# Performance work log

Measured on AMD Instinct MI355X. Metric: run time of the kernel, lower is better.

## Reference

```python
import jax, jax.numpy as jnp
import numpy as np

B, S, D, H, F = 2, 2048, 2048, 16, 6144
HD = D // H  # 128
EPS = 1e-5
NEG = -1e9


def layernorm(x, g, b):
    m = jnp.mean(x, axis=-1, keepdims=True)
    v = jnp.var(x, axis=-1, keepdims=True)
    return (x - m) * jax.lax.rsqrt(v + EPS) * g + b


def setup_inputs() -> dict:
    key = jax.random.key(0)
    ks = jax.random.split(key, 16)
    w = 0.02
    hidden_states = jax.random.normal(ks[0], (B, S, D), jnp.float32)
    # additive causal mask [B,1,S,S]
    causal = jnp.tril(jnp.ones((S, S), jnp.bool_))
    attention_mask = jnp.broadcast_to(jnp.where(causal, 0.0, NEG).astype(jnp.float32)[None, None], (B, 1, S, S))
    # ALiBi position bias [H,S,S]
    slopes = 2.0 ** (-8.0 * (jnp.arange(1, H + 1, dtype=jnp.float32)) / H)
    rel = (jnp.arange(S)[None, :] - jnp.arange(S)[:, None]).astype(jnp.float32)  # j - i (<=0 causal)
    position_bias = slopes[:, None, None] * rel[None]
    params = dict(
        ln1_g=jnp.ones((D,), jnp.float32), ln1_b=jnp.zeros((D,), jnp.float32),
        w_qkv=jax.random.normal(ks[1], (D, 3 * D), jnp.float32) * w,
        b_qkv=jnp.zeros((3 * D,), jnp.float32),
        w_o=jax.random.normal(ks[2], (D, D), jnp.float32) * w,
        b_o=jnp.zeros((D,), jnp.float32),
        ln2_g=jnp.ones((D,), jnp.float32), ln2_b=jnp.zeros((D,), jnp.float32),
        w_fc=jax.random.normal(ks[3], (D, F), jnp.float32) * w,
        b_fc=jnp.zeros((F,), jnp.float32),
        w_fc2=jax.random.normal(ks[4], (D, F), jnp.float32) * w,
        b_fc2=jnp.zeros((F,), jnp.float32),
        w_proj=jax.random.normal(ks[5], (F, D), jnp.float32) * w,
        b_proj=jnp.zeros((D,), jnp.float32),
    )
    return dict(hidden_states=hidden_states, attention_mask=attention_mask,
                position_bias=position_bias, **params)


def reference(hidden_states, attention_mask, position_bias,
              ln1_g, ln1_b, w_qkv, b_qkv, w_o, b_o,
              ln2_g, ln2_b, w_fc, b_fc, w_fc2, b_fc2, w_proj, b_proj):
    residual = hidden_states
    h = layernorm(hidden_states, ln1_g, ln1_b)
    qkv = h @ w_qkv + b_qkv  # [B,S,3D]
    q, k, v = jnp.split(qkv, 3, axis=-1)
    # split heads -> [B,H,S,HD]
    def heads(t):
        return t.reshape(B, S, H, HD).transpose(0, 2, 1, 3)
    q, k, v = heads(q), heads(k), heads(v)
    # muP scaling: attn_scale_power=1.0 -> divide by head_dim
    scores = jnp.einsum('bhqd,bhkd->bhqk', q, k) / jnp.float32(HD)
    scores = scores + attention_mask + position_bias[None]
    probs = jax.nn.softmax(scores, axis=-1)
    ctx = jnp.einsum('bhqk,bhkd->bhqd', probs, v)
    ctx = ctx.transpose(0, 2, 1, 3).reshape(B, S, D)
    attn_out = ctx @ w_o + b_o
    hidden = attn_out + residual
    # SwiGLU MLP
    residual = hidden
    h2 = layernorm(hidden, ln2_g, ln2_b)
    gate = h2 @ w_fc2 + b_fc2
    up = h2 @ w_fc + b_fc
    mlp = (up * jax.nn.silu(gate)) @ w_proj + b_proj
    return mlp + residual
```

## Files before the change

kernel.cpp:

```cpp
#include <hip/hip_runtime.h>
#include <hip/hip_bf16.h>
#include <math.h>

#define DI __device__ __forceinline__

typedef __bf16 bf16x8 __attribute__((ext_vector_type(8)));
typedef float f32x4 __attribute__((ext_vector_type(4)));
typedef short s16x8 __attribute__((ext_vector_type(8)));

DI unsigned short f2bf(float f) {
  unsigned int u = __builtin_bit_cast(unsigned int, f);
  unsigned int r = (u + 0x7fffu + ((u >> 16) & 1u)) >> 16;
  return (unsigned short)r;
}
DI float bf2f(unsigned short h) {
  unsigned int u = ((unsigned int)h) << 16;
  return __builtin_bit_cast(float, u);
}

DI void gload16(const void* g, void* l) {
  __builtin_amdgcn_global_load_lds(
      (const __attribute__((address_space(1))) void*)g,
      (__attribute__((address_space(3))) void*)l, 16, 0, 0);
}

DI unsigned ldsoff(const void* p) {
  return (unsigned)(size_t)(const __attribute__((address_space(3))) void*)p;
}

template <int OFF>
DI bf16x8 ds128(unsigned base) {
  bf16x8 r;
  asm volatile("ds_read_b128 %0, %1 offset:%2" : "=v"(r) : "v"(base), "i"(OFF));
  return r;
}
template <int N>
DI void lgkm() {
  asm volatile("s_waitcnt lgkmcnt(%0)" ::"i"(N));
  __builtin_amdgcn_sched_barrier(0);
}
template <int N>
DI void vmc() {
  asm volatile("s_waitcnt vmcnt(%0)" ::"i"(N));
  __builtin_amdgcn_sched_barrier(0);
}

DI void xcd_map(int BN, int& m0, int& n0) {
  const int nx = gridDim.x;
  int orig = blockIdx.y * nx + blockIdx.x;
  int xcd = orig & 7, k = orig >> 3;
  int xm = xcd >> 2, xn = xcd & 3;
  int nband = nx >> 2;
  m0 = (xm * 8 + (k & 7)) * 256;
  n0 = (xn * nband + (k >> 3)) * BN;
}

__global__ __launch_bounds__(256)
void transpose_cast_f32(const float* __restrict__ in, unsigned short* __restrict__ out,
                        int R, int C) {
  __shared__ unsigned int t[64 * 65];
  const int r0 = blockIdx.y * 64, c0 = blockIdx.x * 64;
  const int tid = threadIdx.x;
#pragma unroll
  for (int p = 0; p < 4; ++p) {
    int e = p * 1024 + tid * 4;
    int r = e >> 6, c = e & 63;
    float4 v = *(const float4*)(in + (size_t)(r0 + r) * C + c0 + c);
    t[r * 65 + c + 0] = f2bf(v.x);
    t[r * 65 + c + 1] = f2bf(v.y);
    t[r * 65 + c + 2] = f2bf(v.z);
    t[r * 65 + c + 3] = f2bf(v.w);
  }
  __syncthreads();
  const int oc = tid >> 2, ch = tid & 3;
  alignas(16) unsigned short vals[16];
#pragma unroll
  for (int j = 0; j < 16; ++j) vals[j] = (unsigned short)t[(ch * 16 + j) * 65 + oc];
  size_t ob = (size_t)(c0 + oc) * R + r0 + ch * 16;
  *(s16x8*)(out + ob) = *(const s16x8*)(vals);
  *(s16x8*)(out + ob + 8) = *(const s16x8*)(vals + 8);
}

__global__ __launch_bounds__(256)
void transpose_v(const unsigned short* __restrict__ qkv, unsigned short* __restrict__ vT) {
  __shared__ unsigned int t[64 * 65];
  const int s0 = blockIdx.x * 64, d0 = blockIdx.y * 64, bh = blockIdx.z;
  const int b = bh >> 4, h = bh & 15;
  const int tid = threadIdx.x;
#pragma unroll
  for (int p = 0; p < 2; ++p) {
    int id = p * 256 + tid;
    int r = id >> 3, c = (id & 7) * 8;
    s16x8 v = *(const s16x8*)(qkv + (size_t)(b * 2048 + s0 + r) * 6144 + 4096 + h * 128 + d0 + c);
#pragma unroll
    for (int j = 0; j < 8; ++j) t[r * 65 + c + j] = (unsigned short)((const unsigned short*)&v)[j];
  }
  __syncthreads();
  const int oc = tid >> 2, ch = tid & 3;
  alignas(16) unsigned short vals[16];
#pragma unroll
  for (int j = 0; j < 16; ++j) vals[j] = (unsigned short)t[(ch * 16 + j) * 65 + oc];
  size_t ob = (size_t)(bh * 128 + d0 + oc) * 2048 + s0 + ch * 16;
  *(s16x8*)(vT + ob) = *(const s16x8*)(vals);
  *(s16x8*)(vT + ob + 8) = *(const s16x8*)(vals + 8);
}

__global__ __launch_bounds__(256)
void ln_kernel(const float* __restrict__ x, const float* __restrict__ g,
               const float* __restrict__ bi, unsigned short* __restrict__ y) {
  __shared__ float red[8];
  const int row = blockIdx.x, tid = threadIdx.x;
  const float* xp = x + (size_t)row * 2048 + tid * 8;
  float4 v0 = *(const float4*)xp;
  float4 v1 = *(const float4*)(xp + 4);
  float v[8] = {v0.x, v0.y, v0.z, v0.w, v1.x, v1.y, v1.z, v1.w};
  float s = 0.f;
#pragma unroll
  for (int j = 0; j < 8; ++j) s += v[j];
#pragma unroll
  for (int d = 1; d < 64; d <<= 1) s += __shfl_xor(s, d);
  if ((tid & 63) == 0) red[tid >> 6] = s;
  __syncthreads();
  float mean = (red[0] + red[1] + red[2] + red[3]) * (1.f / 2048.f);
  float dd[8], sq = 0.f;
#pragma unroll
  for (int j = 0; j < 8; ++j) { dd[j] = v[j] - mean; sq += dd[j] * dd[j]; }
#pragma unroll
  for (int d = 1; d < 64; d <<= 1) sq += __shfl_xor(sq, d);
  if ((tid & 63) == 0) red[4 + (tid >> 6)] = sq;
  __syncthreads();
  float var = (red[4] + red[5] + red[6] + red[7]) * (1.f / 2048.f);
  float rs = rsqrtf(var + 1e-5f);
  float4 g0 = *(const float4*)(g + tid * 8), g1 = *(const float4*)(g + tid * 8 + 4);
  float4 b0 = *(const float4*)(bi + tid * 8), b1 = *(const float4*)(bi + tid * 8 + 4);
  float gg[8] = {g0.x, g0.y, g0.z, g0.w, g1.x, g1.y, g1.z, g1.w};
  float bb[8] = {b0.x, b0.y, b0.z, b0.w, b1.x, b1.y, b1.z, b1.w};
  alignas(16) unsigned short o[8];
#pragma unroll
  for (int j = 0; j < 8; ++j) o[j] = f2bf(dd[j] * rs * gg[j] + bb[j]);
  *(s16x8*)(y + (size_t)row * 2048 + tid * 8) = *(const s16x8*)o;
}

DI void stage_half(const unsigned short* __restrict__ G, int ld, int rbase, int kt,
                   int h, unsigned short* dst, int tid) {
#pragma unroll
  for (int i = 0; i < 2; ++i) {
    int id = i * 512 + tid;
    int rl = id >> 3, sl = id & 7;
    int ss = sl ^ (rl & 7);
    gload16(G + (size_t)(rbase + h * 128 + rl) * ld + kt + ss * 8,
            (char*)dst + h * 16384 + id * 16);
  }
}

#define RDA(dst, B0_, B1_, OFS)                                        \
  dst[0][0] = ds128<(OFS) + 0>(B0_);    dst[0][1] = ds128<(OFS) + 0>(B1_);    \
  dst[1][0] = ds128<(OFS) + 2048>(B0_); dst[1][1] = ds128<(OFS) + 2048>(B1_); \
  dst[2][0] = ds128<(OFS) + 4096>(B0_); dst[2][1] = ds128<(OFS) + 4096>(B1_); \
  dst[3][0] = ds128<(OFS) + 6144>(B0_); dst[3][1] = ds128<(OFS) + 6144>(B1_);

#define RDB(dst, B0_, B1_, OFS)                                        \
  dst[0][0] = ds128<(OFS) + 0>(B0_);    dst[0][1] = ds128<(OFS) + 0>(B1_);    \
  dst[1][0] = ds128<(OFS) + 2048>(B0_); dst[1][1] = ds128<(OFS) + 2048>(B1_);

template <int MODE>
__global__ __launch_bounds__(512, 2)
void gemm256(const unsigned short* __restrict__ A, int lda,
             const unsigned short* __restrict__ B,
             const float* __restrict__ bias,
             const void* __restrict__ resg,
             void* __restrict__ out, int ldc, int K) {
  __shared__ alignas(16) unsigned short As[2][256 * 64];
  __shared__ alignas(16) unsigned short Bs[2][256 * 64];

  const int tid = threadIdx.x;
  const int l = tid & 63, w = tid >> 6;
  const int wr = w >> 2, wc = w & 3;
  const int lr = l & 15, lg = l >> 4;

  int m0, n0;
  xcd_map(256, m0, n0);

  const int NT = K >> 6;

  f32x4 acc[8][4];
  const f32x4 z4 = {0.f, 0.f, 0.f, 0.f};
#pragma unroll
  for (int i = 0; i < 8; ++i)
#pragma unroll
    for (int j = 0; j < 4; ++j) acc[i][j] = z4;

  const int s7 = lr & 7;
  const unsigned swz0 = (unsigned)((lg ^ s7) << 4);
  const unsigned swz1 = (unsigned)(((4 | lg) ^ s7) << 4);
  const unsigned rA = (unsigned)((wr * 128 + lr) * 128);
  const unsigned rB = (unsigned)((wc * 64 + lr) * 128);
  const unsigned aA0 = ldsoff(&As[0][0]) + rA + swz0;
  const unsigned aA1 = ldsoff(&As[0][0]) + rA + swz1;
  const unsigned bA0 = ldsoff(&Bs[0][0]) + rB + swz0;
  const unsigned bA1 = ldsoff(&Bs[0][0]) + rB + swz1;

  stage_half(A, lda, m0, 0, 0, As[0], tid);
  stage_half(A, lda, m0, 0, 1, As[0], tid);
  stage_half(B, K, n0, 0, 0, Bs[0], tid);
  stage_half(B, K, n0, 0, 1, Bs[0], tid);
  if (NT > 1) {
    stage_half(B, K, n0, 64, 0, Bs[1], tid);
    stage_half(B, K, n0, 64, 1, Bs[1], tid);
    stage_half(A, lda, m0, 64, 0, As[1], tid);
    asm volatile("s_waitcnt vmcnt(6)" ::: "memory");
  } else {
    asm volatile("s_waitcnt vmcnt(0)" ::: "memory");
  }
  __builtin_amdgcn_s_barrier();

  for (int t = 0; t < NT; ++t) {
    const unsigned co = (unsigned)((t & 1) * 32768);
    const unsigned a0b = aA0 + co, a1b = aA1 + co;
    const unsigned b0b = bA0 + co, b1b = bA1 + co;
    bf16x8 a0[4][2], a1[4][2], bfr[4][2];

#pragma unroll
    for (int i = 0; i < 4; ++i) {
      a0[i][0] = ds128<0>(a0b + i * 2048);
      a0[i][1] = ds128<0>(a1b + i * 2048);
    }
#pragma unroll
    for (int j = 0; j < 2; ++j) {
      bfr[j][0] = ds128<0>(b0b + j * 2048);
      bfr[j][1] = ds128<0>(b1b + j * 2048);
    }
    if (t + 1 < NT) stage_half(A, lda, m0, (t + 1) * 64, 1, As[(t & 1) ^ 1], tid);
#pragma unroll
    for (int j = 2; j < 4; ++j) {
      bfr[j][0] = ds128<0>(b0b + j * 2048);
      bfr[j][1] = ds128<0>(b1b + j * 2048);
    }
    lgkm<4>();
    __builtin_amdgcn_s_setprio(1);
#pragma unroll
    for (int i = 0; i < 4; ++i)
#pragma unroll
      for (int j = 0; j < 2; ++j)
#pragma unroll
        for (int kk = 0; kk < 2; ++kk)
          acc[i][j] = __builtin_amdgcn_mfma_f32_16x16x32_bf16(a0[i][kk], bfr[j][kk], acc[i][j], 0, 0, 0);
    __builtin_amdgcn_s_setprio(0);
    __builtin_amdgcn_s_barrier();

#pragma unroll
    for (int i = 0; i < 4; ++i) {
      a1[i][0] = ds128<8192>(a0b + i * 2048);
      a1[i][1] = ds128<8192>(a1b + i * 2048);
    }
    lgkm<8>();
    __builtin_amdgcn_s_setprio(1);
#pragma unroll
    for (int i = 0; i < 4; ++i)
#pragma unroll
      for (int j = 2; j < 4; ++j)
#pragma unroll
        for (int kk = 0; kk < 2; ++kk)
          acc[i][j] = __builtin_amdgcn_mfma_f32_16x16x32_bf16(a0[i][kk], bfr[j][kk], acc[i][j], 0, 0, 0);
    __builtin_amdgcn_s_setprio(0);
    __builtin_amdgcn_s_barrier();

    if (t + 2 < NT) stage_half(B, K, n0, (t + 2) * 64, 0, Bs[t & 1], tid);
    lgkm<0>();
    __builtin_amdgcn_s_setprio(1);
#pragma unroll
    for (int i = 0; i < 4; ++i)
#pragma unroll
      for (int j = 0; j < 2; ++j)
#pragma unroll
        for (int kk = 0; kk < 2; ++kk)
          acc[i + 4][j] = __builtin_amdgcn_mfma_f32_16x16x32_bf16(a1[i][kk], bfr[j][kk], acc[i + 4][j], 0, 0, 0);
    __builtin_amdgcn_s_setprio(0);
    __builtin_amdgcn_s_barrier();

    if (t + 2 < NT) {
      stage_half(B, K, n0, (t + 2) * 64, 1, Bs[t & 1], tid);
      stage_half(A, lda, m0, (t + 2) * 64, 0, As[t & 1], tid);
    }
    __builtin_amdgcn_s_setprio(1);
#pragma unroll
    for (int i = 0; i < 4; ++i)
#pragma unroll
      for (int j = 2; j < 4; ++j)
#pragma unroll
        for (int kk = 0; kk < 2; ++kk)
          acc[i + 4][j] = __builtin_amdgcn_mfma_f32_16x16x32_bf16(a1[i][kk], bfr[j][kk], acc[i + 4][j], 0, 0, 0);
    __builtin_amdgcn_s_setprio(0);
    if (t + 2 < NT) { vmc<6>(); } else { vmc<0>(); }
    __builtin_amdgcn_s_barrier();
  }

#pragma unroll
  for (int i = 0; i < 8; ++i) {
    int r0 = m0 + wr * 128 + i * 16 + lg * 4;
#pragma unroll
    for (int j = 0; j < 4; ++j) {
      int col = n0 + wc * 64 + j * 16 + lr;
      float bb = bias[col];
#pragma unroll
      for (int q = 0; q < 4; ++q) {
        size_t off = (size_t)(r0 + q) * ldc + col;
        float v = acc[i][j][q] + bb;
        if (MODE == 0) {
          ((unsigned short*)out)[off] = f2bf(v);
        } else {
          ((float*)out)[off] = v + ((const float*)resg)[off];
        }
      }
    }
  }
}

template <int MODE, bool DUAL>
__global__ __launch_bounds__(512, 2)
void gemm_n128(const unsigned short* __restrict__ A, int lda,
               const unsigned short* __restrict__ B0,
               const unsigned short* __restrict__ B1,
               const float* __restrict__ bias0, const float* __restrict__ bias1,
               const void* __restrict__ resg,
               void* __restrict__ out, int ldc, int K) {
  __shared__ alignas(16) unsigned short As[2][256 * 64];
  __shared__ alignas(16) unsigned short Bs0[2][128 * 64];

  const int tid = threadIdx.x;
  const int l = tid & 63, w = tid >> 6;
  const int wr = w >> 2, wc = w & 3;
  const int lr = l & 15, lg = l >> 4;

  int m0, n0;
  xcd_map(128, m0, n0);

  const int NT = K >> 6;

  f32x4 acc0[8][2];
  const f32x4 z4 = {0.f, 0.f, 0.f, 0.f};
#pragma unroll
  for (int i = 0; i < 8; ++i)
#pragma unroll
    for (int j = 0; j < 2; ++j) acc0[i][j] = z4;

  const int s7 = lr & 7;
  const unsigned swz0 = (unsigned)((lg ^ s7) << 4);
  const unsigned swz1 = (unsigned)(((4 | lg) ^ s7) << 4);
  const unsigned rA = (unsigned)((wr * 128 + lr) * 128);
  const unsigned rB = (unsigned)((wc * 32 + lr) * 128);
  const unsigned aA0 = ldsoff(&As[0][0]) + rA + swz0;
  const unsigned aA1 = ldsoff(&As[0][0]) + rA + swz1;
  const unsigned bA0 = ldsoff(&Bs0[0][0]) + rB + swz0;
  const unsigned bA1 = ldsoff(&Bs0[0][0]) + rB + swz1;

  stage_half(A, lda, m0, 0, 0, As[0], tid);
  stage_half(A, lda, m0, 0, 1, As[0], tid);
  stage_half(B0, K, n0, 0, 0, Bs0[0], tid);
  if (NT > 1) {
    stage_half(B0, K, n0, 64, 0, Bs0[1], tid);
    stage_half(A, lda, m0, 64, 0, As[1], tid);
    asm volatile("s_waitcnt vmcnt(4)" ::: "memory");
  } else {
    asm volatile("s_waitcnt vmcnt(0)" ::: "memory");
  }
  __builtin_amdgcn_s_barrier();

  for (int t = 0; t < NT; ++t) {
    const int cur = t & 1;
    const unsigned ca = aA0 + (unsigned)(cur * 32768);
    const unsigned ca1 = aA1 + (unsigned)(cur * 32768);
    const unsigned cb = bA0 + (unsigned)(cur * 16384);
    const unsigned cb1 = bA1 + (unsigned)(cur * 16384);
    bf16x8 a0[4][2], a1[4][2], b0f[2][2];

#pragma unroll
    for (int i = 0; i < 4; ++i) {
      a0[i][0] = ds128<0>(ca + i * 2048);
      a0[i][1] = ds128<0>(ca1 + i * 2048);
    }
#pragma unroll
    for (int j = 0; j < 2; ++j) {
      b0f[j][0] = ds128<0>(cb + j * 2048);
      b0f[j][1] = ds128<0>(cb1 + j * 2048);
    }
    if (t + 1 < NT) stage_half(A, lda, m0, (t + 1) * 64, 1, As[cur ^ 1], tid);
#pragma unroll
    for (int i = 0; i < 4; ++i) {
      a1[i][0] = ds128<8192>(ca + i * 2048);
      a1[i][1] = ds128<8192>(ca1 + i * 2048);
    }
    lgkm<8>();
    __builtin_amdgcn_s_setprio(1);
#pragma unroll
    for (int i = 0; i < 4; ++i)
#pragma unroll
      for (int j = 0; j < 2; ++j)
#pragma unroll
        for (int kk = 0; kk < 2; ++kk)
          acc0[i][j] = __builtin_amdgcn_mfma_f32_16x16x32_bf16(a0[i][kk], b0f[j][kk], acc0[i][j], 0, 0, 0);
    __builtin_amdgcn_s_setprio(0);
    __builtin_amdgcn_s_barrier();

    if (t + 2 < NT) stage_half(B0, K, n0, (t + 2) * 64, 0, Bs0[cur], tid);
    lgkm<0>();
    if (t + 2 < NT) stage_half(A, lda, m0, (t + 2) * 64, 0, As[cur], tid);
    __builtin_amdgcn_s_setprio(1);
#pragma unroll
    for (int i = 0; i < 4; ++i)
#pragma unroll
      for (int j = 0; j < 2; ++j)
#pragma unroll
        for (int kk = 0; kk < 2; ++kk)
          acc0[i + 4][j] = __builtin_amdgcn_mfma_f32_16x16x32_bf16(a1[i][kk], b0f[j][kk], acc0[i + 4][j], 0, 0, 0);
    __builtin_amdgcn_s_setprio(0);
    if (t + 2 < NT) { vmc<4>(); } else { vmc<0>(); }
    __builtin_amdgcn_s_barrier();
  }

#pragma unroll
  for (int i = 0; i < 8; ++i) {
    int r0 = m0 + wr * 128 + i * 16 + lg * 4;
#pragma unroll
    for (int j = 0; j < 2; ++j) {
      int col = n0 + wc * 32 + j * 16 + lr;
      float bb0 = bias0[col];
#pragma unroll
      for (int q = 0; q < 4; ++q) {
        size_t off = (size_t)(r0 + q) * ldc + col;
        float v = acc0[i][j][q] + bb0;
        ((float*)out)[off] = v + ((const float*)resg)[off];
      }
    }
  }
}

DI void mmq(f32x4 (&acc)[8][2], int io, const bf16x8 (&af)[4][2], const bf16x8 (&bf)[2][2]) {
#pragma unroll
  for (int kk = 0; kk < 2; ++kk)
#pragma unroll
    for (int i = 0; i < 4; ++i)
#pragma unroll
      for (int j = 0; j < 2; ++j)
        acc[io + i][j] = __builtin_amdgcn_mfma_f32_16x16x32_bf16(af[i][kk], bf[j][kk], acc[io + i][j], 0, 0, 0);
}

#define MLP_ITER(t, CUR, A0C, B0C, B1C, A1C, A0N, B0N)                         \
  {                                                                            \
               \
    RDB(B1C, cA0, cA1, (CUR) * 16384);                                         \
    lgkm<4>();                                                                 \
    __builtin_amdgcn_s_setprio(1);                                             \
    mmq(acc0, 0, A0C, B0C);                                                    \
    __builtin_amdgcn_s_setprio(0);                                             \
    __builtin_amdgcn_sched_barrier(0);                                         \
    __builtin_amdgcn_s_barrier();                                              \
      \
    if ((t) + 2 < NT) stage_half(B0, K, n0, ((t) + 2) * 64, 0, Bs0[CUR], tid); \
    RDA(A1C, aA0, aA1, (CUR) * 32768 + 8192);                                  \
    lgkm<8>();                                                                 \
    __builtin_amdgcn_s_setprio(1);                                             \
    mmq(acc1, 0, A0C, B1C);                                                    \
    __builtin_amdgcn_s_setprio(0);                                             \
    if ((t) + 2 < NT) { vmc<2>(); } else { vmc<0>(); }                         \
    __builtin_amdgcn_s_barrier();                                              \
    \
    if ((t) + 2 < NT) stage_half(B1, K, n0, ((t) + 2) * 64, 0, Bs1[CUR], tid); \
    RDA(A0N, aA0, aA1, ((CUR) ^ 1) * 32768);                                   \
    lgkm<8>();                                                                 \
    __builtin_amdgcn_s_setprio(1);                                             \
    mmq(acc0, 4, A1C, B0C);                                                    \
    __builtin_amdgcn_s_setprio(0);                                             \
    __builtin_amdgcn_sched_barrier(0);                                         \
    __builtin_amdgcn_s_barrier();                                              \
     \
    if ((t) + 2 < NT) {                                                        \
      stage_half(A, lda, m0, ((t) + 2) * 64, 0, As[CUR], tid);                 \
      stage_half(A, lda, m0, ((t) + 2) * 64, 1, As[CUR], tid);                 \
    }                                                                          \
    RDB(B0N, bA0, bA1, ((CUR) ^ 1) * 16384);                                   \
    __builtin_amdgcn_sched_barrier(0);                                         \
    __builtin_amdgcn_s_setprio(1);                                             \
    mmq(acc1, 4, A1C, B1C);                                                    \
    __builtin_amdgcn_s_setprio(0);                                             \
    __builtin_amdgcn_sched_barrier(0);                                         \
    __builtin_amdgcn_s_barrier();                                              \
  }

__global__ __launch_bounds__(512, 2)
void gemm_mlp(const unsigned short* __restrict__ A, int lda,
              const unsigned short* __restrict__ B0,
              const unsigned short* __restrict__ B1,
              const float* __restrict__ bias0, const float* __restrict__ bias1,
              unsigned short* __restrict__ out, int ldc, int K) {
  __shared__ alignas(16) unsigned short As[2][256 * 64];
  __shared__ alignas(16) unsigned short Bs0[2][128 * 64];
  __shared__ alignas(16) unsigned short Bs1[2][128 * 64];

  const int tid = threadIdx.x;
  const int l = tid & 63, w = tid >> 6;
  const int wr = w >> 2, wc = w & 3;
  const int lr = l & 15, lg = l >> 4;

  int m0, n0;
  xcd_map(128, m0, n0);
  const int NT = K >> 6;

  f32x4 acc0[8][2], acc1[8][2];
  const f32x4 z4 = {0.f, 0.f, 0.f, 0.f};
#pragma unroll
  for (int i = 0; i < 8; ++i)
#pragma unroll
    for (int j = 0; j < 2; ++j) { acc0[i][j] = z4; acc1[i][j] = z4; }

  const int s7 = lr & 7;
  const unsigned swz0 = (unsigned)((lg ^ s7) << 4);
  const unsigned swz1 = (unsigned)(((4 | lg) ^ s7) << 4);
  const unsigned rA = (unsigned)((wr * 128 + lr) * 128);
  const unsigned rB = (unsigned)((wc * 32 + lr) * 128);
  const unsigned aA0 = ldsoff(&As[0][0]) + rA + swz0;
  const unsigned aA1 = ldsoff(&As[0][0]) + rA + swz1;
  const unsigned bA0 = ldsoff(&Bs0[0][0]) + rB + swz0;
  const unsigned bA1 = ldsoff(&Bs0[0][0]) + rB + swz1;
  const unsigned cA0 = ldsoff(&Bs1[0][0]) + rB + swz0;
  const unsigned cA1 = ldsoff(&Bs1[0][0]) + rB + swz1;

  bf16x8 a0X[4][2], a1X[4][2], b0X[2][2], b1X[2][2];
  bf16x8 a0Y[4][2], a1Y[4][2], b0Y[2][2], b1Y[2][2];

  stage_half(A, lda, m0, 0, 0, As[0], tid);
  stage_half(A, lda, m0, 0, 1, As[0], tid);
  stage_half(B0, K, n0, 0, 0, Bs0[0], tid);
  stage_half(B1, K, n0, 0, 0, Bs1[0], tid);
  stage_half(B0, K, n0, 64, 0, Bs0[1], tid);
  stage_half(B1, K, n0, 64, 0, Bs1[1], tid);
  stage_half(A, lda, m0, 64, 0, As[1], tid);
  stage_half(A, lda, m0, 64, 1, As[1], tid);
  vmc<8>();
  __builtin_amdgcn_s_barrier();
  RDA(a0X, aA0, aA1, 0);
  RDB(b0X, bA0, bA1, 0);

  for (int t = 0; t < NT; t += 2) {
    MLP_ITER(t, 0, a0X, b0X, b1X, a1X, a0Y, b0Y);
    MLP_ITER(t + 1, 1, a0Y, b0Y, b1Y, a1Y, a0X, b0X);
  }

#pragma unroll
  for (int i = 0; i < 8; ++i) {
    int r0 = m0 + wr * 128 + i * 16 + lg * 4;
#pragma unroll
    for (int j = 0; j < 2; ++j) {
      int col = n0 + wc * 32 + j * 16 + lr;
      float bb0 = bias0[col];
      float bb1 = bias1[col];
#pragma unroll
      for (int q = 0; q < 4; ++q) {
        size_t off = (size_t)(r0 + q) * ldc + col;
        float v = acc0[i][j][q] + bb0;
        float gt = acc1[i][j][q] + bb1;
        out[off] = f2bf(v * (gt / (1.f + expf(-gt))));
      }
    }
  }
}

__global__ __launch_bounds__(256, 3)
void attn_kernel(const unsigned short* __restrict__ qkv,
                 const unsigned short* __restrict__ vT,
                 unsigned short* __restrict__ ctx) {
  __shared__ unsigned short Ks[64 * 128];
  __shared__ unsigned short Vs[128 * 64];
  __shared__ unsigned short Ps[4][16 * 80];

  const int g = blockIdx.x;
  const int xcd = g & 7, slot = g >> 3;
  const int bh = xcd * 4 + (slot & 3);
  const int qb = 31 - (slot >> 2);
  const int b = bh >> 4, h = bh & 15;
  const int tid = threadIdx.x, l = tid & 63, w = tid >> 6;
  const int lr = l & 15, lg = l >> 4;
  const float slope2 = exp2f(-0.5f * (float)(h + 1)) * 1.44269504f;
  const float SC2 = 0.0078125f * 1.44269504f;

  const int krow = tid >> 4, kcb = tid & 15;
  const int vrow = tid >> 3, vcb = tid & 7;
  const unsigned short* kbase = qkv + (size_t)(b * 2048 + krow) * 6144 + 2048 + h * 128 + kcb * 8;
  const unsigned short* vbase = vT + (size_t)(bh * 128 + vrow) * 2048 + vcb * 8;
  char* kdst = (char*)Ks + krow * 256 + ((kcb ^ (krow & 7)) << 4);
  char* vdst = (char*)Vs + vrow * 128 + ((vcb ^ (vrow & 7)) << 4);

  int4 kr[4], vr[4];
#pragma unroll
  for (int p = 0; p < 4; ++p) {
    kr[p] = *(const int4*)(kbase + (size_t)p * 16 * 6144);
    vr[p] = *(const int4*)(vbase + (size_t)p * 32 * 2048);
  }

  const int q0 = qb * 64;
  bf16x8 aq[4];
  {
    const unsigned short* qp =
        qkv + (size_t)(b * 2048 + q0 + w * 16 + lr) * 6144 + h * 128 + lg * 8;
#pragma unroll
    for (int kk = 0; kk < 4; ++kk) aq[kk] = *(const bf16x8*)(qp + kk * 32);
  }
  const f32x4 z4 = {0.f, 0.f, 0.f, 0.f};
  f32x4 acc[8];
#pragma unroll
  for (int dt = 0; dt < 8; ++dt) acc[dt] = z4;
  float m_r[4] = {-INFINITY, -INFINITY, -INFINITY, -INFINITY};
  float l_r[4] = {0.f, 0.f, 0.f, 0.f};
  const int ibase = q0 + w * 16 + lg * 4;
  const int nc = qb + 1;

  for (int c = 0; c < nc; ++c) {
    const int kv0 = c * 64;
    __syncthreads();
#pragma unroll
    for (int p = 0; p < 4; ++p) {
      *(int4*)(kdst + p * 4096) = kr[p];
      *(int4*)(vdst + p * 4096) = vr[p];
    }
    __syncthreads();
    if (c + 1 < nc) {
      int nxt = (c + 1) * 64;
#pragma unroll
      for (int p = 0; p < 4; ++p) {
        kr[p] = *(const int4*)(kbase + (size_t)nxt * 6144 + (size_t)p * 16 * 6144);
        vr[p] = *(const int4*)(vbase + nxt + (size_t)p * 32 * 2048);
      }
    }

    f32x4 sc[4];
#pragma unroll
    for (int t = 0; t < 4; ++t) sc[t] = z4;
    __builtin_amdgcn_s_setprio(1);
#pragma unroll
    for (int t = 0; t < 4; ++t) {
#pragma unroll
      for (int kk = 0; kk < 4; ++kk) {
        int row = t * 16 + lr;
        int bo = (row * 256 + kk * 64 + lg * 16) ^ ((row & 7) << 4);
        bf16x8 bk = *(const bf16x8*)((const char*)Ks + bo);
        sc[t] = __builtin_amdgcn_mfma_f32_16x16x32_bf16(aq[kk], bk, sc[t], 0, 0, 0);
      }
    }
    __builtin_amdgcn_s_setprio(0);
    float cmax[4] = {-INFINITY, -INFINITY, -INFINITY, -INFINITY};
#pragma unroll
    for (int t = 0; t < 4; ++t)
#pragma unroll
      for (int q = 0; q < 4; ++q) {
        int j = kv0 + t * 16 + lr;
        int i = ibase + q;
        float s = sc[t][q] * SC2 + slope2 * (float)(j - i);
        if (j > i) s = -1e9f;
        sc[t][q] = s;
        cmax[q] = fmaxf(cmax[q], s);
      }
#pragma unroll
    for (int q = 0; q < 4; ++q) {
      float v = cmax[q];
      v = fmaxf(v, __shfl_xor(v, 1));
      v = fmaxf(v, __shfl_xor(v, 2));
      v = fmaxf(v, __shfl_xor(v, 4));
      v = fmaxf(v, __shfl_xor(v, 8));
      cmax[q] = v;
    }
    float alpha[4], rsum[4];
#pragma unroll
    for (int q = 0; q < 4; ++q) {
      float mn = fmaxf(m_r[q], cmax[q]);
      alpha[q] = exp2f(m_r[q] - mn);
      m_r[q] = mn;
      rsum[q] = 0.f;
    }
#pragma unroll
    for (int t = 0; t < 4; ++t)
#pragma unroll
      for (int q = 0; q < 4; ++q) {
        float p = exp2f(sc[t][q] - m_r[q]);
        rsum[q] += p;
        sc[t][q] = p;
      }
#pragma unroll
    for (int q = 0; q < 4; ++q) {
      float v = rsum[q];
      v += __shfl_xor(v, 1);
      v += __shfl_xor(v, 2);
      v += __shfl_xor(v, 4);
      v += __shfl_xor(v, 8);
      l_r[q] = l_r[q] * alpha[q] + v;
    }
#pragma unroll
    for (int dt = 0; dt < 8; ++dt)
#pragma unroll
      for (int q = 0; q < 4; ++q) acc[dt][q] *= alpha[q];
#pragma unroll
    for (int t = 0; t < 4; ++t)
#pragma unroll
      for (int q = 0; q < 4; ++q)
        Ps[w][(lg * 4 + q) * 80 + t * 16 + lr] = f2bf(sc[t][q]);
    __builtin_amdgcn_s_setprio(1);
#pragma unroll
    for (int kc = 0; kc < 2; ++kc) {
      bf16x8 ap = *(const bf16x8*)(&Ps[w][lr * 80 + kc * 32 + lg * 8]);
#pragma unroll
      for (int dt = 0; dt < 8; ++dt) {
        int row = dt * 16 + lr;
        int bo = (row * 128 + kc * 64 + lg * 16) ^ ((row & 7) << 4);
        bf16x8 bv = *(const bf16x8*)((const char*)Vs + bo);
        acc[dt] = __builtin_amdgcn_mfma_f32_16x16x32_bf16(ap, bv, acc[dt], 0, 0, 0);
      }
    }
    __builtin_amdgcn_s_setprio(0);
  }

  float inv4[4];
#pragma unroll
  for (int q = 0; q < 4; ++q) inv4[q] = 1.f / l_r[q];
  const int rr = l >> 2, c4 = l & 3;
#pragma unroll
  for (int chv = 0; chv < 2; ++chv) {
#pragma unroll
    for (int q = 0; q < 4; ++q) {
      int rl = lg * 4 + q;
#pragma unroll
      for (int dt = 0; dt < 4; ++dt)
        Ps[w][rl * 80 + dt * 16 + lr] = f2bf(acc[chv * 4 + dt][q] * inv4[q]);
    }
    const unsigned short* srow = &Ps[w][rr * 80 + c4 * 8];
    size_t gb = (size_t)(b * 2048 + q0 + w * 16 + rr) * 2048 + h * 128 + chv * 64 + c4 * 8;
    *(s16x8*)(ctx + gb) = *(const s16x8*)(srow);
    *(s16x8*)(ctx + gb + 32) = *(const s16x8*)(srow + 32);
  }
}

extern "C" void kernel_launch(void* const* d_in, const int* in_sizes, int n_in,
                              void* d_out, int out_size, void* d_ws, size_t ws_size,
                              hipStream_t stream) {
  const float* hs   = (const float*)d_in[0];
  const float* ln1g = (const float*)d_in[3];
  const float* ln1b = (const float*)d_in[4];
  const float* wqkv = (const float*)d_in[5];
  const float* bqkv = (const float*)d_in[6];
  const float* wo   = (const float*)d_in[7];
  const float* bo   = (const float*)d_in[8];
  const float* ln2g = (const float*)d_in[9];
  const float* ln2b = (const float*)d_in[10];
  const float* wfc  = (const float*)d_in[11];
  const float* bfc  = (const float*)d_in[12];
  const float* wfc2 = (const float*)d_in[13];
  const float* bfc2 = (const float*)d_in[14];
  const float* wpj  = (const float*)d_in[15];
  const float* bpj  = (const float*)d_in[16];

  char* ws = (char*)d_ws;
  unsigned short* woT   = (unsigned short*)(ws + 0);
  unsigned short* wfcT  = (unsigned short*)(ws + 8388608);
  unsigned short* wfc2T = (unsigned short*)(ws + 33554432);
  unsigned short* hbuf  = (unsigned short*)(ws + 58720256);
  unsigned short* qkvb  = (unsigned short*)(ws + 75497472);
  unsigned short* wqkvT = (unsigned short*)(ws + 125829120);
  unsigned short* vTb   = (unsigned short*)(ws + 150994944);
  unsigned short* ctxb  = (unsigned short*)(ws + 167772160);
  unsigned short* wpjT  = wqkvT;
  float* outf = (float*)d_out;

  dim3 blk(256), blk512(512);
  transpose_cast_f32<<<dim3(96, 32), blk, 0, stream>>>(wqkv, wqkvT, 2048, 6144);
  transpose_cast_f32<<<dim3(32, 32), blk, 0, stream>>>(wo, woT, 2048, 2048);
  transpose_cast_f32<<<dim3(96, 32), blk, 0, stream>>>(wfc, wfcT, 2048, 6144);
  transpose_cast_f32<<<dim3(96, 32), blk, 0, stream>>>(wfc2, wfc2T, 2048, 6144);
  ln_kernel<<<dim3(4096), blk, 0, stream>>>(hs, ln1g, ln1b, hbuf);
  gemm256<0><<<dim3(24, 16), blk512, 0, stream>>>(hbuf, 2048, wqkvT, bqkv, nullptr,
                                                  qkvb, 6144, 2048);
  transpose_v<<<dim3(32, 2, 32), blk, 0, stream>>>(qkvb, vTb);
  transpose_cast_f32<<<dim3(32, 96), blk, 0, stream>>>(wpj, wpjT, 6144, 2048);
  attn_kernel<<<dim3(1024), blk, 0, stream>>>(qkvb, vTb, ctxb);
  gemm_n128<1, false><<<dim3(16, 16), blk512, 0, stream>>>(
      ctxb, 2048, woT, nullptr, bo, nullptr, hs, d_out, 2048, 2048);
  ln_kernel<<<dim3(4096), blk, 0, stream>>>(outf, ln2g, ln2b, hbuf);
  gemm_mlp<<<dim3(48, 16), blk512, 0, stream>>>(
      hbuf, 2048, wfcT, wfc2T, bfc, bfc2, qkvb, 6144, 2048);
  gemm_n128<1, false><<<dim3(16, 16), blk512, 0, stream>>>(
      qkvb, 6144, wpjT, nullptr, bpj, nullptr, outf, d_out, 2048, 6144);
}
```

Before: 723.6 us.

## Pair causal query blocks per workgroup and double-buffer K/V tiles in LDS

Each attention workgroup now processes two query blocks (pid and 31-pid), so every workgroup handles 33 KV chunks and the causal work is balanced, with half as many workgroups launched. K/V tiles are double-buffered in LDS, so the store of the next tile happens after the QK MFMAs and needs one barrier per chunk instead of two. Registers prefetch the tile two chunks ahead. LDS use doubles and launch bounds drop to 2 blocks per CU, which lowers occupancy. The grid also becomes smaller relative to the CU count.

```diff
diff --git a/kernel.cpp b/kernel.cpp
--- a/kernel.cpp
+++ b/kernel.cpp
@@ -565,18 +565,18 @@
   }
 }
 
-__global__ __launch_bounds__(256, 3)
+__global__ __launch_bounds__(256, 2)
 void attn_kernel(const unsigned short* __restrict__ qkv,
                  const unsigned short* __restrict__ vT,
                  unsigned short* __restrict__ ctx) {
-  __shared__ unsigned short Ks[64 * 128];
-  __shared__ unsigned short Vs[128 * 64];
+  __shared__ unsigned short Ks[2][64 * 128];
+  __shared__ unsigned short Vs[2][128 * 64];
   __shared__ unsigned short Ps[4][16 * 80];
 
   const int g = blockIdx.x;
   const int xcd = g & 7, slot = g >> 3;
   const int bh = xcd * 4 + (slot & 3);
-  const int qb = 31 - (slot >> 2);
+  const int pid = slot >> 2;
   const int b = bh >> 4, h = bh & 15;
   const int tid = threadIdx.x, l = tid & 63, w = tid >> 6;
   const int lr = l & 15, lg = l >> 4;
@@ -587,8 +587,10 @@
   const int vrow = tid >> 3, vcb = tid & 7;
   const unsigned short* kbase = qkv + (size_t)(b * 2048 + krow) * 6144 + 2048 + h * 128 + kcb * 8;
   const unsigned short* vbase = vT + (size_t)(bh * 128 + vrow) * 2048 + vcb * 8;
-  char* kdst = (char*)Ks + krow * 256 + ((kcb ^ (krow & 7)) << 4);
-  char* vdst = (char*)Vs + vrow * 128 + ((vcb ^ (vrow & 7)) << 4);
+  const int koff = krow * 256 + ((kcb ^ (krow & 7)) << 4);
+  const int voff = vrow * 128 + ((vcb ^ (vrow & 7)) << 4);
+
+  const int nc0 = pid + 1;
 
   int4 kr[4], vr[4];
 #pragma unroll
@@ -596,144 +598,172 @@
     kr[p] = *(const int4*)(kbase + (size_t)p * 16 * 6144);
     vr[p] = *(const int4*)(vbase + (size_t)p * 32 * 2048);
   }
-
-  const int q0 = qb * 64;
-  bf16x8 aq[4];
+#pragma unroll
+  for (int p = 0; p < 4; ++p) {
+    *(int4*)((char*)Ks[0] + koff + p * 4096) = kr[p];
+    *(int4*)((char*)Vs[0] + voff + p * 4096) = vr[p];
+  }
   {
-    const unsigned short* qp =
-        qkv + (size_t)(b * 2048 + q0 + w * 16 + lr) * 6144 + h * 128 + lg * 8;
-#pragma unroll
-    for (int kk = 0; kk < 4; ++kk) aq[kk] = *(const bf16x8*)(qp + kk * 32);
-  }
-  const f32x4 z4 = {0.f, 0.f, 0.f, 0.f};
-  f32x4 acc[8];
-#pragma unroll
-  for (int dt = 0; dt < 8; ++dt) acc[dt] = z4;
-  float m_r[4] = {-INFINITY, -INFINITY, -INFINITY, -INFINITY};
-  float l_r[4] = {0.f, 0.f, 0.f, 0.f};
-  const int ibase = q0 + w * 16 + lg * 4;
-  const int nc = qb + 1;
-
-  for (int c = 0; c < nc; ++c) {
-    const int kv0 = c * 64;
-    __syncthreads();
+    int nk = ((1 < nc0) ? 1 : 0) * 64;
 #pragma unroll
     for (int p = 0; p < 4; ++p) {
-      *(int4*)(kdst + p * 4096) = kr[p];
-      *(int4*)(vdst + p * 4096) = vr[p];
-    }
-    __syncthreads();
-    if (c + 1 < nc) {
-      int nxt = (c + 1) * 64;
-#pragma unroll
-      for (int p = 0; p < 4; ++p) {
-        kr[p] = *(const int4*)(kbase + (size_t)nxt * 6144 + (size_t)p * 16 * 6144);
-        vr[p] = *(const int4*)(vbase + nxt + (size_t)p * 32 * 2048);
-      }
-    }
-
-    f32x4 sc[4];
-#pragma unroll
-    for (int t = 0; t < 4; ++t) sc[t] = z4;
-    __builtin_amdgcn_s_setprio(1);
-#pragma unroll
-    for (int t = 0; t < 4; ++t) {
-#pragma unroll
-      for (int kk = 0; kk < 4; ++kk) {
-        int row = t * 16 + lr;
-        int bo = (row * 256 + kk * 64 + lg * 16) ^ ((row & 7) << 4);
-        bf16x8 bk = *(const bf16x8*)((const char*)Ks + bo);
-        sc[t] = __builtin_amdgcn_mfma_f32_16x16x32_bf16(aq[kk], bk, sc[t], 0, 0, 0);
-      }
-    }
-    __builtin_amdgcn_s_setprio(0);
-    float cmax[4] = {-INFINITY, -INFINITY, -INFINITY, -INFINITY};
-#pragma unroll
-    for (int t = 0; t < 4; ++t)
+      kr[p] = *(const int4*)(kbase + (size_t)nk * 6144 + (size_t)p * 16 * 6144);
+      vr[p] = *(const int4*)(vbase + nk + (size_t)p * 32 * 2048);
+    }
+  }
+  __syncthreads();
+
+  for (int tq = 0; tq < 2; ++tq) {
+    const int qb = tq ? (31 - pid) : pid;
+    const int q0 = qb * 64;
+    const int nc = qb + 1;
+    const int gb0 = tq ? nc0 : 0;
+    bf16x8 aq[4];
+    {
+      const unsigned short* qp =
+          qkv + (size_t)(b * 2048 + q0 + w * 16 + lr) * 6144 + h * 128 + lg * 8;
+#pragma unroll
+      for (int kk = 0; kk < 4; ++kk) aq[kk] = *(const bf16x8*)(qp + kk * 32);
+    }
+    const f32x4 z4 = {0.f, 0.f, 0.f, 0.f};
+    f32x4 acc[8];
+#pragma unroll
+    for (int dt = 0; dt < 8; ++dt) acc[dt] = z4;
+    float m_r[4] = {-INFINITY, -INFINITY, -INFINITY, -INFINITY};
+    float l_r[4] = {0.f, 0.f, 0.f, 0.f};
+    const int ibase = q0 + w * 16 + lg * 4;
+
+    for (int c = 0; c < nc; ++c) {
+      const int gi = gb0 + c;
+      const int cur = gi & 1;
+      const char* Kc = (const char*)Ks[cur];
+      const char* Vc = (const char*)Vs[cur];
+      const int kv0 = c * 64;
+
+      f32x4 sc[4];
+#pragma unroll
+      for (int t = 0; t < 4; ++t) sc[t] = z4;
+      __builtin_amdgcn_s_setprio(1);
+#pragma unroll
+      for (int t = 0; t < 4; ++t) {
+#pragma unroll
+        for (int kk = 0; kk < 4; ++kk) {
+          int row = t * 16 + lr;
+          int bo = (row * 256 + kk * 64 + lg * 16) ^ ((row & 7) << 4);
+          bf16x8 bk = *(const bf16x8*)(Kc + bo);
+          sc[t] = __builtin_amdgcn_mfma_f32_16x16x32_bf16(aq[kk], bk, sc[t], 0, 0, 0);
+        }
+      }
+      __builtin_amdgcn_s_setprio(0);
+
+      if (gi + 1 < 33) {
+        char* kd = (char*)Ks[cur ^ 1] + koff;
+        char* vd = (char*)Vs[cur ^ 1] + voff;
+#pragma unroll
+        for (int p = 0; p < 4; ++p) {
+          *(int4*)(kd + p * 4096) = kr[p];
+          *(int4*)(vd + p * 4096) = vr[p];
+        }
+      }
+      if (gi + 2 < 33) {
+        int i2 = gi + 2;
+        int nk = ((i2 < nc0) ? i2 : i2 - nc0) * 64;
+#pragma unroll
+        for (int p = 0; p < 4; ++p) {
+          kr[p] = *(const int4*)(kbase + (size_t)nk * 6144 + (size_t)p * 16 * 6144);
+          vr[p] = *(const int4*)(vbase + nk + (size_t)p * 32 * 2048);
+        }
+      }
+
+      float cmax[4] = {-INFINITY, -INFINITY, -INFINITY, -INFINITY};
+#pragma unroll
+      for (int t = 0; t < 4; ++t)
+#pragma unroll
+        for (int q = 0; q < 4; ++q) {
+          int j = kv0 + t * 16 + lr;
+          int i = ibase + q;
+          float s = sc[t][q] * SC2 + slope2 * (float)(j - i);
+          if (j > i) s = -1e9f;
+          sc[t][q] = s;
+          cmax[q] = fmaxf(cmax[q], s);
+        }
 #pragma unroll
       for (int q = 0; q < 4; ++q) {
-        int j = kv0 + t * 16 + lr;
-        int i = ibase + q;
-        float s = sc[t][q] * SC2 + slope2 * (float)(j - i);
-        if (j > i) s = -1e9f;
-        sc[t][q] = s;
-        cmax[q] = fmaxf(cmax[q], s);
-      }
-#pragma unroll
-    for (int q = 0; q < 4; ++q) {
-      float v = cmax[q];
-      v = fmaxf(v, __shfl_xor(v, 1));
-      v = fmaxf(v, __shfl_xor(v, 2));
-      v = fmaxf(v, __shfl_xor(v, 4));
-      v = fmaxf(v, __shfl_xor(v, 8));
-      cmax[q] = v;
-    }
-    float alpha[4], rsum[4];
-#pragma unroll
-    for (int q = 0; q < 4; ++q) {
-      float mn = fmaxf(m_r[q], cmax[q]);
-      alpha[q] = exp2f(m_r[q] - mn);
-      m_r[q] = mn;
-      rsum[q] = 0.f;
-    }
-#pragma unroll
-    for (int t = 0; t < 4; ++t)
+        float v = cmax[q];
+        v = fmaxf(v, __shfl_xor(v, 1));
+        v = fmaxf(v, __shfl_xor(v, 2));
+        v = fmaxf(v, __shfl_xor(v, 4));
+        v = fmaxf(v, __shfl_xor(v, 8));
+        cmax[q] = v;
+      }
+      float alpha[4], rsum[4];
 #pragma unroll
       for (int q = 0; q < 4; ++q) {
-        float p = exp2f(sc[t][q] - m_r[q]);
-        rsum[q] += p;
-        sc[t][q] = p;
-      }
-#pragma unroll
-    for (int q = 0; q < 4; ++q) {
-      float v = rsum[q];
-      v += __shfl_xor(v, 1);
-      v += __shfl_xor(v, 2);
-      v += __shfl_xor(v, 4);
-      v += __shfl_xor(v, 8);
-      l_r[q] = l_r[q] * alpha[q] + v;
-    }
-#pragma unroll
-    for (int dt = 0; dt < 8; ++dt)
-#pragma unroll
-      for (int q = 0; q < 4; ++q) acc[dt][q] *= alpha[q];
-#pragma unroll
-    for (int t = 0; t < 4; ++t)
-#pragma unroll
-      for (int q = 0; q < 4; ++q)
-        Ps[w][(lg * 4 + q) * 80 + t * 16 + lr] = f2bf(sc[t][q]);
-    __builtin_amdgcn_s_setprio(1);
-#pragma unroll
-    for (int kc = 0; kc < 2; ++kc) {
-      bf16x8 ap = *(const bf16x8*)(&Ps[w][lr * 80 + kc * 32 + lg * 8]);
-#pragma unroll
-      for (int dt = 0; dt < 8; ++dt) {
-        int row = dt * 16 + lr;
-        int bo = (row * 128 + kc * 64 + lg * 16) ^ ((row & 7) << 4);
-        bf16x8 bv = *(const bf16x8*)((const char*)Vs + bo);
-        acc[dt] = __builtin_amdgcn_mfma_f32_16x16x32_bf16(ap, bv, acc[dt], 0, 0, 0);
-      }
-    }
-    __builtin_amdgcn_s_setprio(0);
-  }
-
-  float inv4[4];
-#pragma unroll
-  for (int q = 0; q < 4; ++q) inv4[q] = 1.f / l_r[q];
-  const int rr = l >> 2, c4 = l & 3;
-#pragma unroll
-  for (int chv = 0; chv < 2; ++chv) {
-#pragma unroll
-    for (int q = 0; q < 4; ++q) {
-      int rl = lg * 4 + q;
-#pragma unroll
-      for (int dt = 0; dt < 4; ++dt)
-        Ps[w][rl * 80 + dt * 16 + lr] = f2bf(acc[chv * 4 + dt][q] * inv4[q]);
-    }
-    const unsigned short* srow = &Ps[w][rr * 80 + c4 * 8];
-    size_t gb = (size_t)(b * 2048 + q0 + w * 16 + rr) * 2048 + h * 128 + chv * 64 + c4 * 8;
-    *(s16x8*)(ctx + gb) = *(const s16x8*)(srow);
-    *(s16x8*)(ctx + gb + 32) = *(const s16x8*)(srow + 32);
+        float mn = fmaxf(m_r[q], cmax[q]);
+        alpha[q] = exp2f(m_r[q] - mn);
+        m_r[q] = mn;
+        rsum[q] = 0.f;
+      }
+#pragma unroll
+      for (int t = 0; t < 4; ++t)
+#pragma unroll
+        for (int q = 0; q < 4; ++q) {
+          float p = exp2f(sc[t][q] - m_r[q]);
+          rsum[q] += p;
+          sc[t][q] = p;
+        }
+#pragma unroll
+      for (int q = 0; q < 4; ++q) {
+        float v = rsum[q];
+        v += __shfl_xor(v, 1);
+        v += __shfl_xor(v, 2);
+        v += __shfl_xor(v, 4);
+        v += __shfl_xor(v, 8);
+        l_r[q] = l_r[q] * alpha[q] + v;
+      }
+#pragma unroll
+      for (int dt = 0; dt < 8; ++dt)
+#pragma unroll
+        for (int q = 0; q < 4; ++q) acc[dt][q] *= alpha[q];
+#pragma unroll
+      for (int t = 0; t < 4; ++t)
+#pragma unroll
+        for (int q = 0; q < 4; ++q)
+          Ps[w][(lg * 4 + q) * 80 + t * 16 + lr] = f2bf(sc[t][q]);
+      __builtin_amdgcn_s_setprio(1);
+#pragma unroll
+      for (int kc = 0; kc < 2; ++kc) {
+        bf16x8 ap = *(const bf16x8*)(&Ps[w][lr * 80 + kc * 32 + lg * 8]);
+#pragma unroll
+        for (int dt = 0; dt < 8; ++dt) {
+          int row = dt * 16 + lr;
+          int bo = (row * 128 + kc * 64 + lg * 16) ^ ((row & 7) << 4);
+          bf16x8 bv = *(const bf16x8*)(Vc + bo);
+          acc[dt] = __builtin_amdgcn_mfma_f32_16x16x32_bf16(ap, bv, acc[dt], 0, 0, 0);
+        }
+      }
+      __builtin_amdgcn_s_setprio(0);
+      __syncthreads();
+    }
+
+    float inv4[4];
+#pragma unroll
+    for (int q = 0; q < 4; ++q) inv4[q] = 1.f / l_r[q];
+    const int rr = l >> 2, c4 = l & 3;
+#pragma unroll
+    for (int chv = 0; chv < 2; ++chv) {
+#pragma unroll
+      for (int q = 0; q < 4; ++q) {
+        int rl = lg * 4 + q;
+#pragma unroll
+        for (int dt = 0; dt < 4; ++dt)
+          Ps[w][rl * 80 + dt * 16 + lr] = f2bf(acc[chv * 4 + dt][q] * inv4[q]);
+      }
+      const unsigned short* srow = &Ps[w][rr * 80 + c4 * 8];
+      size_t gb = (size_t)(b * 2048 + q0 + w * 16 + rr) * 2048 + h * 128 + chv * 64 + c4 * 8;
+      *(s16x8*)(ctx + gb) = *(const s16x8*)(srow);
+      *(s16x8*)(ctx + gb + 32) = *(const s16x8*)(srow + 32);
+    }
   }
 }
 
@@ -778,7 +808,7 @@
                                                   qkvb, 6144, 2048);
   transpose_v<<<dim3(32, 2, 32), blk, 0, stream>>>(qkvb, vTb);
   transpose_cast_f32<<<dim3(32, 96), blk, 0, stream>>>(wpj, wpjT, 6144, 2048);
-  attn_kernel<<<dim3(1024), blk, 0, stream>>>(qkvb, vTb, ctxb);
+  attn_kernel<<<dim3(512), blk, 0, stream>>>(qkvb, vTb, ctxb);
   gemm_n128<1, false><<<dim3(16, 16), blk512, 0, stream>>>(
       ctxb, 2048, woT, nullptr, bo, nullptr, hs, d_out, 2048, 2048);
   ln_kernel<<<dim3(4096), blk, 0, stream>>>(outf, ln2g, ln2b, hbuf);
```

Result: no change. 715.7 us (-1.1%).
